# Kernel tuning notes

Measured on AMD Instinct MI355X. Metric: run time of the kernel, lower is better.

Reference implementation:

```python
import jax, jax.numpy as jnp
import numpy as np

N_NODES = 100000
N_EDGES = 1600000
D = 128        # in_dim == hidden_dim (forced by x_j + xe in message)
C = 64         # num_classes
G = 128        # number of graphs in the batch
BN_EPS = 1e-5


def setup_inputs() -> dict:
    key = jax.random.key(0)
    ks = jax.random.split(key, 14)
    s = 0.05
    inp = {
        "x": jax.random.normal(ks[0], (N_NODES, D), dtype=jnp.float32),
        "xe": jax.random.normal(ks[1], (N_EDGES, D), dtype=jnp.float32),
        "edge_index": jax.random.randint(ks[2], (2, N_EDGES), 0, N_NODES, dtype=jnp.int32),
        "batch": jnp.sort(jax.random.randint(ks[3], (N_NODES,), 0, G, dtype=jnp.int32)),
        # layer 0 MySAGEConv params
        "Wl0": jax.random.normal(ks[4], (D, D), dtype=jnp.float32) * s,
        "bl0": jnp.zeros((D,), dtype=jnp.float32),
        "Wr0": jax.random.normal(ks[5], (D, D), dtype=jnp.float32) * s,
        # layer 1 MySAGEConv params
        "Wl1": jax.random.normal(ks[6], (D, D), dtype=jnp.float32) * s,
        "bl1": jnp.zeros((D,), dtype=jnp.float32),
        "Wr1": jax.random.normal(ks[7], (D, D), dtype=jnp.float32) * s,
        # BatchNorm (only applied after non-final layers -> layer 0)
        "gamma0": jnp.ones((D,), dtype=jnp.float32),
        "beta0": jnp.zeros((D,), dtype=jnp.float32),
        # readout projection
        "Wp": jax.random.normal(ks[8], (C, D), dtype=jnp.float32) * s,
        "bp": jnp.zeros((C,), dtype=jnp.float32),
    }
    return inp


def _segment_mean(vals, idx, num_segments):
    s = jax.ops.segment_sum(vals, idx, num_segments=num_segments)
    cnt = jax.ops.segment_sum(jnp.ones((vals.shape[0],), vals.dtype), idx,
                              num_segments=num_segments)
    return s / jnp.clip(cnt, 1.0)[:, None]


def _my_sage_conv(h, xe, src, dst, Wl, bl, Wr):
    # message: relu(x_j + xe); aggregate: scatter-mean at dst; then lin_l + lin_r
    msg = jax.nn.relu(h[src] + xe)                       # [E, D]
    agg = _segment_mean(msg, dst, N_NODES)               # [N, D]
    return agg @ Wl.T + bl + h @ Wr.T


def _batchnorm_train(h, gamma, beta):
    mu = jnp.mean(h, axis=0)
    var = jnp.var(h, axis=0)
    return gamma * (h - mu) * jax.lax.rsqrt(var + BN_EPS) + beta


def reference(x, xe, edge_index, batch,
              Wl0, bl0, Wr0, Wl1, bl1, Wr1,
              gamma0, beta0, Wp, bp):
    src, dst = edge_index[0], edge_index[1]
    # layer 0: conv -> BN -> ReLU
    h = _my_sage_conv(x, xe, src, dst, Wl0, bl0, Wr0)
    h = jax.nn.relu(_batchnorm_train(h, gamma0, beta0))
    # layer 1 (last): conv only
    h = _my_sage_conv(h, xe, src, dst, Wl1, bl1, Wr1)
    # graph readout (global mean pool over pre-proj node features)
    g = _segment_mean(h, batch, G)                       # [G, D]
    # readout projection on nodes
    h = jax.nn.relu(h) @ Wp.T + bp                       # [N, C]
    return h, g
```

## Files before the change

kernel.cpp:

```cpp
#include <hip/hip_runtime.h>

#define N_NODES 100000
#define N_EDGES 1600000
#define DIM 128
#define NCLS 64
#define NG 128
#define BN_EPS 1e-5f

typedef __attribute__((ext_vector_type(8))) short s16x8;
typedef __attribute__((ext_vector_type(4))) float f32x4;
#define MFMA_BF16 __builtin_amdgcn_mfma_f32_16x16x32_bf16

__device__ __forceinline__ unsigned short f2b(float x) {
    unsigned u = __float_as_uint(x);
    return (unsigned short)((u + 0x7FFFu + ((u >> 16) & 1u)) >> 16);
}
__device__ __forceinline__ float b2f(unsigned short s) {
    return __uint_as_float(((unsigned)s) << 16);
}
__device__ __forceinline__ float4 bexp4(ushort4 u) {
    float4 f;
    f.x = b2f(u.x); f.y = b2f(u.y); f.z = b2f(u.z); f.w = b2f(u.w);
    return f;
}

__device__ __forceinline__ void f2hl8(float4 v0, float4 v1, s16x8& h8, s16x8& l8) {
    float vv[8] = {v0.x, v0.y, v0.z, v0.w, v1.x, v1.y, v1.z, v1.w};
#pragma unroll
    for (int i = 0; i < 8; ++i) {
        unsigned u = __float_as_uint(vv[i]);
        short h = (short)(u >> 16);
        float r = vv[i] - __uint_as_float(u & 0xFFFF0000u);
        short l = (short)(__float_as_uint(r) >> 16);
        h8[i] = h;
        l8[i] = l;
    }
}

__device__ __forceinline__ float4 relu4(float4 v) {
    v.x = fmaxf(v.x, 0.f); v.y = fmaxf(v.y, 0.f);
    v.z = fmaxf(v.z, 0.f); v.w = fmaxf(v.w, 0.f);
    return v;
}

__global__ void k_cvt(const float* __restrict__ in, unsigned short* __restrict__ out,
                      int n8) {
    int i = blockIdx.x * 256 + threadIdx.x;
    if (i >= n8) return;
    float4 a = reinterpret_cast<const float4*>(in)[(size_t)i * 2];
    float4 b = reinterpret_cast<const float4*>(in)[(size_t)i * 2 + 1];
    ushort4 oa, ob;
    oa.x = f2b(a.x); oa.y = f2b(a.y); oa.z = f2b(a.z); oa.w = f2b(a.w);
    ob.x = f2b(b.x); ob.y = f2b(b.y); ob.z = f2b(b.z); ob.w = f2b(b.w);
    reinterpret_cast<ushort4*>(out)[(size_t)i * 2] = oa;
    reinterpret_cast<ushort4*>(out)[(size_t)i * 2 + 1] = ob;
}

__global__ void k_hist(const int* __restrict__ dst, int* __restrict__ cnt) {
    int e = blockIdx.x * 256 + threadIdx.x;
    if (e < N_EDGES) atomicAdd(&cnt[dst[e]], 1);
}

__global__ void k_scan1(const int* __restrict__ cnt, int* __restrict__ rowptr,
                        int* __restrict__ bsums) {
    __shared__ int sd[1024];
    int tid = threadIdx.x;
    int i = blockIdx.x * 1024 + tid;
    int v = (i < N_NODES) ? cnt[i] : 0;
    sd[tid] = v;
    __syncthreads();
    for (int off = 1; off < 1024; off <<= 1) {
        int t2 = (tid >= off) ? sd[tid - off] : 0;
        __syncthreads();
        sd[tid] += t2;
        __syncthreads();
    }
    if (i < N_NODES) rowptr[i] = sd[tid] - v;
    if (tid == 1023) bsums[blockIdx.x] = sd[tid];
}

__global__ void k_scan2(int* __restrict__ bsums, int nb) {
    __shared__ int sd[128];
    int t = threadIdx.x;
    int v = (t < nb) ? bsums[t] : 0;
    sd[t] = v;
    __syncthreads();
    for (int off = 1; off < 128; off <<= 1) {
        int u = (t >= off) ? sd[t - off] : 0;
        __syncthreads();
        sd[t] += u;
        __syncthreads();
    }
    if (t < nb) bsums[t] = sd[t] - v;
}

__global__ void k_scan3(int* __restrict__ rowptr, const int* __restrict__ bsums,
                        int* __restrict__ wcur) {
    int i = blockIdx.x * 1024 + threadIdx.x;
    if (i < N_NODES) {
        int v = rowptr[i] + bsums[blockIdx.x];
        rowptr[i] = v;
        wcur[i] = v;
    }
    if (i == N_NODES - 1) rowptr[N_NODES] = N_EDGES;
}

__global__ void k_scatter(const int* __restrict__ src, const int* __restrict__ dst,
                          int* __restrict__ wcur, int2* __restrict__ esort) {
    int e = blockIdx.x * 256 + threadIdx.x;
    if (e < N_EDGES) {
        int d = dst[e];
        int p = atomicAdd(&wcur[d], 1);
        esort[p] = make_int2(e, src[e]);
    }
}

template <int MODE>
__global__ __launch_bounds__(256) void k_agg(
        const unsigned short* __restrict__ Fb, const float* __restrict__ xe,
        unsigned short* __restrict__ xe_s,
        const int* __restrict__ rowptr, const int2* __restrict__ esort,
        float* __restrict__ agg, const float* __restrict__ bnsc) {
    int wid = (blockIdx.x * 256 + threadIdx.x) >> 6;
    int lane = threadIdx.x & 63;
    if (wid >= N_NODES) return;
    int half = lane >> 5;
    int l = lane & 31;
    int p0 = rowptr[wid], p1 = rowptr[wid + 1];
    if (p0 == p1) {
        if (half == 0) {
            float4 z = make_float4(0.f, 0.f, 0.f, 0.f);
            *reinterpret_cast<float4*>(&agg[(size_t)wid * DIM + l * 4]) = z;
        }
        return;
    }
    float4 sc, sh;
    if (MODE != 0) {
        sc = *reinterpret_cast<const float4*>(&bnsc[l * 4]);
        sh = *reinterpret_cast<const float4*>(&bnsc[DIM + l * 4]);
    }
    float4 acc = make_float4(0.f, 0.f, 0.f, 0.f);
    for (int p = p0; p < p1; p += 8) {
#pragma unroll
        for (int j = 0; j < 4; ++j) {
            int q = p + j * 2 + half;
            int qc = min(q, p1 - 1);
            int2 es = esort[qc];
            float4 a = bexp4(*reinterpret_cast<const ushort4*>(
                &Fb[(size_t)es.y * DIM + l * 4]));
            float4 b;
            if (MODE == 1) {
                b = bexp4(*reinterpret_cast<const ushort4*>(
                    &xe_s[(size_t)qc * DIM + l * 4]));
            } else {
                b = *reinterpret_cast<const float4*>(
                    &xe[(size_t)es.x * DIM + l * 4]);
            }
            if (MODE != 0) {
                a.x = fmaxf(a.x * sc.x + sh.x, 0.f);
                a.y = fmaxf(a.y * sc.y + sh.y, 0.f);
                a.z = fmaxf(a.z * sc.z + sh.z, 0.f);
                a.w = fmaxf(a.w * sc.w + sh.w, 0.f);
            }
            if (q < p1) {
                if (MODE == 0) {
                    ushort4 o;
                    o.x = f2b(b.x); o.y = f2b(b.y);
                    o.z = f2b(b.z); o.w = f2b(b.w);
                    *reinterpret_cast<ushort4*>(&xe_s[(size_t)qc * DIM + l * 4]) = o;
                }
                acc.x += fmaxf(a.x + b.x, 0.f);
                acc.y += fmaxf(a.y + b.y, 0.f);
                acc.z += fmaxf(a.z + b.z, 0.f);
                acc.w += fmaxf(a.w + b.w, 0.f);
            }
        }
    }
    acc.x += __shfl_xor(acc.x, 32);
    acc.y += __shfl_xor(acc.y, 32);
    acc.z += __shfl_xor(acc.z, 32);
    acc.w += __shfl_xor(acc.w, 32);
    if (half == 0) {
        float s = 1.f / (float)(p1 - p0);
        acc.x *= s; acc.y *= s; acc.z *= s; acc.w *= s;
        *reinterpret_cast<float4*>(&agg[(size_t)wid * DIM + l * 4]) = acc;
    }
}

__global__ void k_wprep_all(const float* __restrict__ Wl0, const float* __restrict__ Wr0,
                            const float* __restrict__ Wl1, const float* __restrict__ Wr1,
                            const float* __restrict__ Wp,
                            short* __restrict__ fWl0h, short* __restrict__ fWl0l,
                            short* __restrict__ fWr0h, short* __restrict__ fWr0l,
                            short* __restrict__ fWl1h, short* __restrict__ fWl1l,
                            short* __restrict__ fWr1h, short* __restrict__ fWr1l,
                            short* __restrict__ fWph, short* __restrict__ fWpl) {
    int b = blockIdx.x;
    const float* W; short* hi; short* lo; int ct;
    if (b < 8)       { W = Wl0; hi = fWl0h; lo = fWl0l; ct = b; }
    else if (b < 16) { W = Wr0; hi = fWr0h; lo = fWr0l; ct = b - 8; }
    else if (b < 24) { W = Wl1; hi = fWl1h; lo = fWl1l; ct = b - 16; }
    else if (b < 32) { W = Wr1; hi = fWr1h; lo = fWr1l; ct = b - 24; }
    else             { W = Wp;  hi = fWph;  lo = fWpl;  ct = b - 32; }
    int tt = threadIdx.x;
    int lane = tt & 63, ks = (tt >> 6) & 3;
    int row = ct * 16 + (lane & 15);
    int k0 = ks * 32 + ((lane >> 4) << 3);
    float4 v0 = *reinterpret_cast<const float4*>(&W[(size_t)row * DIM + k0]);
    float4 v1 = *reinterpret_cast<const float4*>(&W[(size_t)row * DIM + k0 + 4]);
    s16x8 h8, l8;
    f2hl8(v0, v1, h8, l8);
    int t = ct * 256 + ks * 64 + lane;
    *reinterpret_cast<s16x8*>(&hi[(size_t)t * 8]) = h8;
    *reinterpret_cast<s16x8*>(&lo[(size_t)t * 8]) = l8;
}

__global__ __launch_bounds__(256) void k_gemm2(
        const float* __restrict__ A, const unsigned short* __restrict__ Bbf,
        const short* __restrict__ fW1h, const short* __restrict__ fW1l,
        const short* __restrict__ fW2h, const short* __restrict__ fW2l,
        const float* __restrict__ bias, float* __restrict__ OUTf,
        unsigned short* __restrict__ OUTb,
        float* __restrict__ bnacc, const float* __restrict__ bnsc,
        int doBN, int bnB) {
    int t = threadIdx.x, w = t >> 6, l = t & 63;
    int n0 = blockIdx.x * 128;
    int r = l & 15, kh = l >> 4;
    int row0 = n0 + w * 16 + r;
    int row1 = row0 + 64;
    int n_0 = min(row0, N_NODES - 1);
    int n_1 = min(row1, N_NODES - 1);

    f32x4 acc0[8], acc1[8];
#pragma unroll
    for (int ct = 0; ct < 8; ++ct) {
        acc0[ct] = (f32x4){0.f, 0.f, 0.f, 0.f};
        acc1[ct] = (f32x4){0.f, 0.f, 0.f, 0.f};
    }
    const s16x8* w1h = (const s16x8*)fW1h;
    const s16x8* w1l = (const s16x8*)fW1l;
    const s16x8* w2h = (const s16x8*)fW2h;
    const s16x8* w2l = (const s16x8*)fW2l;

#pragma unroll
    for (int ks = 0; ks < 4; ++ks) {
        int kb = ks * 32 + kh * 8;
        float4 va0 = *reinterpret_cast<const float4*>(&A[(size_t)n_0 * DIM + kb]);
        float4 va1 = *reinterpret_cast<const float4*>(&A[(size_t)n_0 * DIM + kb + 4]);
        float4 wa0 = *reinterpret_cast<const float4*>(&A[(size_t)n_1 * DIM + kb]);
        float4 wa1 = *reinterpret_cast<const float4*>(&A[(size_t)n_1 * DIM + kb + 4]);
        s16x8 b0 = *reinterpret_cast<const s16x8*>(&Bbf[(size_t)n_0 * DIM + kb]);
        s16x8 b1 = *reinterpret_cast<const s16x8*>(&Bbf[(size_t)n_1 * DIM + kb]);
        if (bnB) {
            float4 sc0 = *reinterpret_cast<const float4*>(&bnsc[kb]);
            float4 sh0 = *reinterpret_cast<const float4*>(&bnsc[DIM + kb]);
            float4 sc1 = *reinterpret_cast<const float4*>(&bnsc[kb + 4]);
            float4 sh1 = *reinterpret_cast<const float4*>(&bnsc[DIM + kb + 4]);
            float scv[8] = {sc0.x, sc0.y, sc0.z, sc0.w, sc1.x, sc1.y, sc1.z, sc1.w};
            float shv[8] = {sh0.x, sh0.y, sh0.z, sh0.w, sh1.x, sh1.y, sh1.z, sh1.w};
#pragma unroll
            for (int i = 0; i < 8; ++i) {
                float v = b2f((unsigned short)b0[i]);
                b0[i] = (short)f2b(fmaxf(v * scv[i] + shv[i], 0.f));
                v = b2f((unsigned short)b1[i]);
                b1[i] = (short)f2b(fmaxf(v * scv[i] + shv[i], 0.f));
            }
        }
        s16x8 a0h, a0l, a1h, a1l;
        f2hl8(va0, va1, a0h, a0l);
        f2hl8(wa0, wa1, a1h, a1l);
        int fb = ks * 64 + l;
#pragma unroll
        for (int ct = 0; ct < 8; ++ct) {
            int fi = ct * 256 + fb;
            s16x8 wh1 = w1h[fi], wl1 = w1l[fi];
            s16x8 wh2 = w2h[fi], wl2 = w2l[fi];
            acc0[ct] = MFMA_BF16(a0h, wh1, acc0[ct], 0, 0, 0);
            acc0[ct] = MFMA_BF16(a0h, wl1, acc0[ct], 0, 0, 0);
            acc0[ct] = MFMA_BF16(a0l, wh1, acc0[ct], 0, 0, 0);
            acc0[ct] = MFMA_BF16(b0, wh2, acc0[ct], 0, 0, 0);
            acc0[ct] = MFMA_BF16(b0, wl2, acc0[ct], 0, 0, 0);
            acc1[ct] = MFMA_BF16(a1h, wh1, acc1[ct], 0, 0, 0);
            acc1[ct] = MFMA_BF16(a1h, wl1, acc1[ct], 0, 0, 0);
            acc1[ct] = MFMA_BF16(a1l, wh1, acc1[ct], 0, 0, 0);
            acc1[ct] = MFMA_BF16(b1, wh2, acc1[ct], 0, 0, 0);
            acc1[ct] = MFMA_BF16(b1, wl2, acc1[ct], 0, 0, 0);
        }
    }

    float p1s[8], p2s[8];
    int col0 = l & 15;
    int nb0 = n0 + w * 16 + (kh << 2);
    int nb1 = nb0 + 64;
#pragma unroll
    for (int ct = 0; ct < 8; ++ct) {
        float bj = bias[ct * 16 + col0];
        float s1 = 0.f, s2 = 0.f;
#pragma unroll
        for (int rr = 0; rr < 4; ++rr) {
            int n = nb0 + rr;
            float h = acc0[ct][rr] + bj;
            if (n < N_NODES) {
                if (OUTb) OUTb[(size_t)n * DIM + ct * 16 + col0] = f2b(h);
                else      OUTf[(size_t)n * DIM + ct * 16 + col0] = h;
                s1 += h; s2 += h * h;
            }
            n = nb1 + rr;
            h = acc1[ct][rr] + bj;
            if (n < N_NODES) {
                if (OUTb) OUTb[(size_t)n * DIM + ct * 16 + col0] = f2b(h);
                else      OUTf[(size_t)n * DIM + ct * 16 + col0] = h;
                s1 += h; s2 += h * h;
            }
        }
        p1s[ct] = s1; p2s[ct] = s2;
    }
    if (doBN) {
        __shared__ float red1[512];
        __shared__ float red2[512];
#pragma unroll
        for (int ct = 0; ct < 8; ++ct) {
            p1s[ct] += __shfl_xor(p1s[ct], 16);
            p1s[ct] += __shfl_xor(p1s[ct], 32);
            p2s[ct] += __shfl_xor(p2s[ct], 16);
            p2s[ct] += __shfl_xor(p2s[ct], 32);
        }
        if (l < 16) {
#pragma unroll
            for (int ct = 0; ct < 8; ++ct) {
                red1[w * 128 + ct * 16 + l] = p1s[ct];
                red2[w * 128 + ct * 16 + l] = p2s[ct];
            }
        }
        __syncthreads();
        if (t < 128) {
            float s1 = red1[t] + red1[128 + t] + red1[256 + t] + red1[384 + t];
            float s2 = red2[t] + red2[128 + t] + red2[256 + t] + red2[384 + t];
            atomicAdd(&bnacc[t], s1);
            atomicAdd(&bnacc[128 + t], s2);
        }
    }
}

__global__ void k_bnfinal(const float* __restrict__ bnacc, const float* __restrict__ gamma,
                          const float* __restrict__ beta, float* __restrict__ bnsc) {
    int d = threadIdx.x;
    if (d < DIM) {
        float mu = bnacc[d] / (float)N_NODES;
        float var = bnacc[128 + d] / (float)N_NODES - mu * mu;
        float rstd = rsqrtf(var + BN_EPS);
        float sc = gamma[d] * rstd;
        bnsc[d] = sc;
        bnsc[128 + d] = beta[d] - mu * sc;
    }
}

__global__ void k_pool(const float* __restrict__ H1, const int* __restrict__ batch,
                       float* __restrict__ gout) {
    __shared__ float red[4][128];
    int g = blockIdx.x;
    int t = threadIdx.x;
    int d = t & 127;
    int sl = t >> 7;
    int lo = 0, hi = N_NODES;
    while (lo < hi) { int m = (lo + hi) >> 1; if (batch[m] < g) lo = m + 1; else hi = m; }
    int s = lo;
    lo = 0; hi = N_NODES;
    while (lo < hi) { int m = (lo + hi) >> 1; if (batch[m] < g + 1) lo = m + 1; else hi = m; }
    int e = lo;
    float sum = 0.f;
    for (int n = s + sl; n < e; n += 4) sum += H1[(size_t)n * DIM + d];
    red[sl][d] = sum;
    __syncthreads();
    if (t < 128) {
        float tot = red[0][d] + red[1][d] + red[2][d] + red[3][d];
        gout[g * DIM + d] = tot / (float)max(e - s, 1);
    }
}

__global__ __launch_bounds__(256) void k_proj(
        const float* __restrict__ H1, const short* __restrict__ fWph,
        const short* __restrict__ fWpl, const float* __restrict__ bp,
        float* __restrict__ OUT) {
    int t = threadIdx.x, w = t >> 6, l = t & 63;
    int n0 = blockIdx.x * 128;
    int r = l & 15, kh = l >> 4;
    int row0 = n0 + w * 16 + r;
    int row1 = row0 + 64;
    int n_0 = min(row0, N_NODES - 1);
    int n_1 = min(row1, N_NODES - 1);
    f32x4 acc0[4], acc1[4];
#pragma unroll
    for (int ct = 0; ct < 4; ++ct) {
        acc0[ct] = (f32x4){0.f, 0.f, 0.f, 0.f};
        acc1[ct] = (f32x4){0.f, 0.f, 0.f, 0.f};
    }
    const s16x8* wph = (const s16x8*)fWph;
    const s16x8* wpl = (const s16x8*)fWpl;
#pragma unroll
    for (int ks = 0; ks < 4; ++ks) {
        int kb = ks * 32 + kh * 8;
        float4 va0 = relu4(*reinterpret_cast<const float4*>(&H1[(size_t)n_0 * DIM + kb]));
        float4 va1 = relu4(*reinterpret_cast<const float4*>(&H1[(size_t)n_0 * DIM + kb + 4]));
        float4 wa0 = relu4(*reinterpret_cast<const float4*>(&H1[(size_t)n_1 * DIM + kb]));
        float4 wa1 = relu4(*reinterpret_cast<const float4*>(&H1[(size_t)n_1 * DIM + kb + 4]));
        s16x8 a0h, a0l, a1h, a1l;
        f2hl8(va0, va1, a0h, a0l);
        f2hl8(wa0, wa1, a1h, a1l);
        int fb = ks * 64 + l;
#pragma unroll
        for (int ct = 0; ct < 4; ++ct) {
            int fi = ct * 256 + fb;
            s16x8 wh = wph[fi], wl = wpl[fi];
            acc0[ct] = MFMA_BF16(a0h, wh, acc0[ct], 0, 0, 0);
            acc0[ct] = MFMA_BF16(a0h, wl, acc0[ct], 0, 0, 0);
            acc0[ct] = MFMA_BF16(a0l, wh, acc0[ct], 0, 0, 0);
            acc1[ct] = MFMA_BF16(a1h, wh, acc1[ct], 0, 0, 0);
            acc1[ct] = MFMA_BF16(a1h, wl, acc1[ct], 0, 0, 0);
            acc1[ct] = MFMA_BF16(a1l, wh, acc1[ct], 0, 0, 0);
        }
    }
    int col0 = l & 15;
    int nb0 = n0 + w * 16 + (kh << 2);
    int nb1 = nb0 + 64;
#pragma unroll
    for (int ct = 0; ct < 4; ++ct) {
        float bj = bp[ct * 16 + col0];
#pragma unroll
        for (int rr = 0; rr < 4; ++rr) {
            int n = nb0 + rr;
            if (n < N_NODES)
                OUT[(size_t)n * NCLS + ct * 16 + col0] = acc0[ct][rr] + bj;
            n = nb1 + rr;
            if (n < N_NODES)
                OUT[(size_t)n * NCLS + ct * 16 + col0] = acc1[ct][rr] + bj;
        }
    }
}

extern "C" void kernel_launch(void* const* d_in, const int* in_sizes, int n_in,
                              void* d_out, int out_size, void* d_ws, size_t ws_size,
                              hipStream_t stream) {
    (void)in_sizes; (void)n_in; (void)out_size;
    const float* x     = (const float*)d_in[0];
    const float* xe    = (const float*)d_in[1];
    const int*   eidx  = (const int*)d_in[2];
    const int*   batch = (const int*)d_in[3];
    const float* Wl0   = (const float*)d_in[4];
    const float* bl0   = (const float*)d_in[5];
    const float* Wr0   = (const float*)d_in[6];
    const float* Wl1   = (const float*)d_in[7];
    const float* bl1   = (const float*)d_in[8];
    const float* Wr1   = (const float*)d_in[9];
    const float* gamma0 = (const float*)d_in[10];
    const float* beta0  = (const float*)d_in[11];
    const float* Wp    = (const float*)d_in[12];
    const float* bp    = (const float*)d_in[13];
    const int* srcp = eidx;
    const int* dstp = eidx + N_EDGES;

    char* ws = (char*)d_ws;
    size_t off = 0;
    auto carve = [&](size_t bytes) {
        void* p = ws + off;
        off = (off + bytes + 255) & ~(size_t)255;
        return p;
    };
    int*   cnt    = (int*)carve((size_t)N_NODES * 4);
    int*   rowptr = (int*)carve((size_t)(N_NODES + 1) * 4);
    int*   wcur   = (int*)carve((size_t)N_NODES * 4);
    int*   bsums  = (int*)carve(128 * 4);
    float* bnacc  = (float*)carve(256 * 4);
    float* bnsc   = (float*)carve(256 * 4);
    int2*  esort  = (int2*)carve((size_t)N_EDGES * 8);
    float* AGG    = (float*)carve((size_t)N_NODES * DIM * 4);
    float* H1     = (float*)carve((size_t)N_NODES * DIM * 4);
    unsigned short* x_bf = (unsigned short*)carve((size_t)N_NODES * DIM * 2);
    unsigned short* H_bf = (unsigned short*)carve((size_t)N_NODES * DIM * 2);
    short* fWl0h = (short*)carve(16384 * 2);
    short* fWl0l = (short*)carve(16384 * 2);
    short* fWr0h = (short*)carve(16384 * 2);
    short* fWr0l = (short*)carve(16384 * 2);
    short* fWl1h = (short*)carve(16384 * 2);
    short* fWl1l = (short*)carve(16384 * 2);
    short* fWr1h = (short*)carve(16384 * 2);
    short* fWr1l = (short*)carve(16384 * 2);
    short* fWph  = (short*)carve(8192 * 2);
    short* fWpl  = (short*)carve(8192 * 2);

    size_t xes_bytes = (size_t)N_EDGES * DIM * 2;
    int seq = (off + xes_bytes + 256 <= ws_size) ? 1 : 0;
    unsigned short* xe_s = seq ? (unsigned short*)carve(xes_bytes) : nullptr;

    float* out_h = (float*)d_out;
    float* out_g = out_h + (size_t)N_NODES * NCLS;

    hipMemsetAsync(cnt, 0, (size_t)N_NODES * 4, stream);
    hipMemsetAsync(bnacc, 0, 256 * 4, stream);

    k_wprep_all<<<36, 256, 0, stream>>>(Wl0, Wr0, Wl1, Wr1, Wp,
                                        fWl0h, fWl0l, fWr0h, fWr0l,
                                        fWl1h, fWl1l, fWr1h, fWr1l,
                                        fWph, fWpl);
    k_cvt<<<(N_NODES * DIM / 8 + 255) / 256, 256, 0, stream>>>(x, x_bf,
                                                               N_NODES * DIM / 8);

    int nb = (N_NODES + 1023) / 1024;
    k_hist<<<(N_EDGES + 255) / 256, 256, 0, stream>>>(dstp, cnt);
    k_scan1<<<nb, 1024, 0, stream>>>(cnt, rowptr, bsums);
    k_scan2<<<1, 128, 0, stream>>>(bsums, nb);
    k_scan3<<<nb, 1024, 0, stream>>>(rowptr, bsums, wcur);
    k_scatter<<<(N_EDGES + 255) / 256, 256, 0, stream>>>(srcp, dstp, wcur, esort);

    int ablocks = (N_NODES * 64 + 255) / 256;
    int gblocks = (N_NODES + 127) / 128;

    if (seq)
        k_agg<0><<<ablocks, 256, 0, stream>>>(x_bf, xe, xe_s, rowptr, esort, AGG, bnsc);
    else
        k_agg<2><<<ablocks, 256, 0, stream>>>(x_bf, xe, nullptr, rowptr, esort, AGG, bnsc);
    k_gemm2<<<gblocks, 256, 0, stream>>>(AGG, x_bf, fWl0h, fWl0l, fWr0h, fWr0l,
                                         bl0, nullptr, H_bf, bnacc, bnsc, 1, 0);
    k_bnfinal<<<1, 128, 0, stream>>>(bnacc, gamma0, beta0, bnsc);

    if (seq)
        k_agg<1><<<ablocks, 256, 0, stream>>>(H_bf, xe, xe_s, rowptr, esort, AGG, bnsc);
    else
        k_agg<2><<<ablocks, 256, 0, stream>>>(H_bf, xe, nullptr, rowptr, esort, AGG, bnsc);
    k_gemm2<<<gblocks, 256, 0, stream>>>(AGG, H_bf, fWl1h, fWl1l, fWr1h, fWr1l,
                                         bl1, H1, nullptr, bnacc, bnsc, 0, 1);

    k_pool<<<NG, 512, 0, stream>>>(H1, batch, out_g);
    k_proj<<<gblocks, 256, 0, stream>>>(H1, fWph, fWpl, bp, out_h);
}
```

Measured before the change: 866.1 us.

## Store aggregates and final hidden features in bf16; fuse setup kernels

```diff
diff --git a/kernel.cpp b/kernel.cpp
--- a/kernel.cpp
+++ b/kernel.cpp
@@ -37,28 +37,50 @@
     }
 }
 
-__device__ __forceinline__ float4 relu4(float4 v) {
-    v.x = fmaxf(v.x, 0.f); v.y = fmaxf(v.y, 0.f);
-    v.z = fmaxf(v.z, 0.f); v.w = fmaxf(v.w, 0.f);
-    return v;
-}
-
-__global__ void k_cvt(const float* __restrict__ in, unsigned short* __restrict__ out,
-                      int n8) {
-    int i = blockIdx.x * 256 + threadIdx.x;
-    if (i >= n8) return;
-    float4 a = reinterpret_cast<const float4*>(in)[(size_t)i * 2];
-    float4 b = reinterpret_cast<const float4*>(in)[(size_t)i * 2 + 1];
-    ushort4 oa, ob;
-    oa.x = f2b(a.x); oa.y = f2b(a.y); oa.z = f2b(a.z); oa.w = f2b(a.w);
-    ob.x = f2b(b.x); ob.y = f2b(b.y); ob.z = f2b(b.z); ob.w = f2b(b.w);
-    reinterpret_cast<ushort4*>(out)[(size_t)i * 2] = oa;
-    reinterpret_cast<ushort4*>(out)[(size_t)i * 2 + 1] = ob;
-}
-
-__global__ void k_hist(const int* __restrict__ dst, int* __restrict__ cnt) {
-    int e = blockIdx.x * 256 + threadIdx.x;
-    if (e < N_EDGES) atomicAdd(&cnt[dst[e]], 1);
+__global__ __launch_bounds__(256) void k_mega0(
+        const float* __restrict__ Wl0, const float* __restrict__ Wr0,
+        const float* __restrict__ Wl1, const float* __restrict__ Wr1,
+        const float* __restrict__ Wp,
+        short* __restrict__ fWl0h, short* __restrict__ fWl0l,
+        short* __restrict__ fWr0h, short* __restrict__ fWr0l,
+        short* __restrict__ fWl1h, short* __restrict__ fWl1l,
+        short* __restrict__ fWr1h, short* __restrict__ fWr1l,
+        short* __restrict__ fWph, short* __restrict__ fWpl,
+        const float* __restrict__ x, unsigned short* __restrict__ x_bf,
+        const int* __restrict__ dst, int* __restrict__ cnt) {
+    int b = blockIdx.x;
+    if (b < 36) {
+        const float* W; short* hi; short* lo; int ct;
+        if (b < 8)       { W = Wl0; hi = fWl0h; lo = fWl0l; ct = b; }
+        else if (b < 16) { W = Wr0; hi = fWr0h; lo = fWr0l; ct = b - 8; }
+        else if (b < 24) { W = Wl1; hi = fWl1h; lo = fWl1l; ct = b - 16; }
+        else if (b < 32) { W = Wr1; hi = fWr1h; lo = fWr1l; ct = b - 24; }
+        else             { W = Wp;  hi = fWph;  lo = fWpl;  ct = b - 32; }
+        if (b >= 32 && ct >= 4) return;
+        int tt = threadIdx.x;
+        int lane = tt & 63, ks = (tt >> 6) & 3;
+        int row = ct * 16 + (lane & 15);
+        int k0 = ks * 32 + ((lane >> 4) << 3);
+        float4 v0 = *reinterpret_cast<const float4*>(&W[(size_t)row * DIM + k0]);
+        float4 v1 = *reinterpret_cast<const float4*>(&W[(size_t)row * DIM + k0 + 4]);
+        s16x8 h8, l8;
+        f2hl8(v0, v1, h8, l8);
+        int t = ct * 256 + ks * 64 + lane;
+        *reinterpret_cast<s16x8*>(&hi[(size_t)t * 8]) = h8;
+        *reinterpret_cast<s16x8*>(&lo[(size_t)t * 8]) = l8;
+    } else if (b < 36 + 6250) {
+        int i = (b - 36) * 256 + threadIdx.x;
+        float4 a = reinterpret_cast<const float4*>(x)[(size_t)i * 2];
+        float4 c = reinterpret_cast<const float4*>(x)[(size_t)i * 2 + 1];
+        ushort4 oa, ob;
+        oa.x = f2b(a.x); oa.y = f2b(a.y); oa.z = f2b(a.z); oa.w = f2b(a.w);
+        ob.x = f2b(c.x); ob.y = f2b(c.y); ob.z = f2b(c.z); ob.w = f2b(c.w);
+        reinterpret_cast<ushort4*>(x_bf)[(size_t)i * 2] = oa;
+        reinterpret_cast<ushort4*>(x_bf)[(size_t)i * 2 + 1] = ob;
+    } else {
+        int e = (b - 36 - 6250) * 256 + threadIdx.x;
+        atomicAdd(&cnt[dst[e]], 1);
+    }
 }
 
 __global__ void k_scan1(const int* __restrict__ cnt, int* __restrict__ rowptr,
@@ -120,7 +142,7 @@
         const unsigned short* __restrict__ Fb, const float* __restrict__ xe,
         unsigned short* __restrict__ xe_s,
         const int* __restrict__ rowptr, const int2* __restrict__ esort,
-        float* __restrict__ agg, const float* __restrict__ bnsc) {
+        unsigned short* __restrict__ agg, const float* __restrict__ bnsc) {
     int wid = (blockIdx.x * 256 + threadIdx.x) >> 6;
     int lane = threadIdx.x & 63;
     if (wid >= N_NODES) return;
@@ -129,8 +151,8 @@
     int p0 = rowptr[wid], p1 = rowptr[wid + 1];
     if (p0 == p1) {
         if (half == 0) {
-            float4 z = make_float4(0.f, 0.f, 0.f, 0.f);
-            *reinterpret_cast<float4*>(&agg[(size_t)wid * DIM + l * 4]) = z;
+            ushort4 z = make_ushort4(0, 0, 0, 0);
+            *reinterpret_cast<ushort4*>(&agg[(size_t)wid * DIM + l * 4]) = z;
         }
         return;
     }
@@ -182,45 +204,18 @@
     acc.w += __shfl_xor(acc.w, 32);
     if (half == 0) {
         float s = 1.f / (float)(p1 - p0);
-        acc.x *= s; acc.y *= s; acc.z *= s; acc.w *= s;
-        *reinterpret_cast<float4*>(&agg[(size_t)wid * DIM + l * 4]) = acc;
-    }
-}
-
-__global__ void k_wprep_all(const float* __restrict__ Wl0, const float* __restrict__ Wr0,
-                            const float* __restrict__ Wl1, const float* __restrict__ Wr1,
-                            const float* __restrict__ Wp,
-                            short* __restrict__ fWl0h, short* __restrict__ fWl0l,
-                            short* __restrict__ fWr0h, short* __restrict__ fWr0l,
-                            short* __restrict__ fWl1h, short* __restrict__ fWl1l,
-                            short* __restrict__ fWr1h, short* __restrict__ fWr1l,
-                            short* __restrict__ fWph, short* __restrict__ fWpl) {
-    int b = blockIdx.x;
-    const float* W; short* hi; short* lo; int ct;
-    if (b < 8)       { W = Wl0; hi = fWl0h; lo = fWl0l; ct = b; }
-    else if (b < 16) { W = Wr0; hi = fWr0h; lo = fWr0l; ct = b - 8; }
-    else if (b < 24) { W = Wl1; hi = fWl1h; lo = fWl1l; ct = b - 16; }
-    else if (b < 32) { W = Wr1; hi = fWr1h; lo = fWr1l; ct = b - 24; }
-    else             { W = Wp;  hi = fWph;  lo = fWpl;  ct = b - 32; }
-    int tt = threadIdx.x;
-    int lane = tt & 63, ks = (tt >> 6) & 3;
-    int row = ct * 16 + (lane & 15);
-    int k0 = ks * 32 + ((lane >> 4) << 3);
-    float4 v0 = *reinterpret_cast<const float4*>(&W[(size_t)row * DIM + k0]);
-    float4 v1 = *reinterpret_cast<const float4*>(&W[(size_t)row * DIM + k0 + 4]);
-    s16x8 h8, l8;
-    f2hl8(v0, v1, h8, l8);
-    int t = ct * 256 + ks * 64 + lane;
-    *reinterpret_cast<s16x8*>(&hi[(size_t)t * 8]) = h8;
-    *reinterpret_cast<s16x8*>(&lo[(size_t)t * 8]) = l8;
+        ushort4 o;
+        o.x = f2b(acc.x * s); o.y = f2b(acc.y * s);
+        o.z = f2b(acc.z * s); o.w = f2b(acc.w * s);
+        *reinterpret_cast<ushort4*>(&agg[(size_t)wid * DIM + l * 4]) = o;
+    }
 }
 
 __global__ __launch_bounds__(256) void k_gemm2(
-        const float* __restrict__ A, const unsigned short* __restrict__ Bbf,
+        const unsigned short* __restrict__ Abf, const unsigned short* __restrict__ Bbf,
         const short* __restrict__ fW1h, const short* __restrict__ fW1l,
         const short* __restrict__ fW2h, const short* __restrict__ fW2l,
-        const float* __restrict__ bias, float* __restrict__ OUTf,
-        unsigned short* __restrict__ OUTb,
+        const float* __restrict__ bias, unsigned short* __restrict__ OUTb,
         float* __restrict__ bnacc, const float* __restrict__ bnsc,
         int doBN, int bnB) {
     int t = threadIdx.x, w = t >> 6, l = t & 63;
@@ -245,10 +240,8 @@
 #pragma unroll
     for (int ks = 0; ks < 4; ++ks) {
         int kb = ks * 32 + kh * 8;
-        float4 va0 = *reinterpret_cast<const float4*>(&A[(size_t)n_0 * DIM + kb]);
-        float4 va1 = *reinterpret_cast<const float4*>(&A[(size_t)n_0 * DIM + kb + 4]);
-        float4 wa0 = *reinterpret_cast<const float4*>(&A[(size_t)n_1 * DIM + kb]);
-        float4 wa1 = *reinterpret_cast<const float4*>(&A[(size_t)n_1 * DIM + kb + 4]);
+        s16x8 a0 = *reinterpret_cast<const s16x8*>(&Abf[(size_t)n_0 * DIM + kb]);
+        s16x8 a1 = *reinterpret_cast<const s16x8*>(&Abf[(size_t)n_1 * DIM + kb]);
         s16x8 b0 = *reinterpret_cast<const s16x8*>(&Bbf[(size_t)n_0 * DIM + kb]);
         s16x8 b1 = *reinterpret_cast<const s16x8*>(&Bbf[(size_t)n_1 * DIM + kb]);
         if (bnB) {
@@ -266,23 +259,18 @@
                 b1[i] = (short)f2b(fmaxf(v * scv[i] + shv[i], 0.f));
             }
         }
-        s16x8 a0h, a0l, a1h, a1l;
-        f2hl8(va0, va1, a0h, a0l);
-        f2hl8(wa0, wa1, a1h, a1l);
         int fb = ks * 64 + l;
 #pragma unroll
         for (int ct = 0; ct < 8; ++ct) {
             int fi = ct * 256 + fb;
             s16x8 wh1 = w1h[fi], wl1 = w1l[fi];
             s16x8 wh2 = w2h[fi], wl2 = w2l[fi];
-            acc0[ct] = MFMA_BF16(a0h, wh1, acc0[ct], 0, 0, 0);
-            acc0[ct] = MFMA_BF16(a0h, wl1, acc0[ct], 0, 0, 0);
-            acc0[ct] = MFMA_BF16(a0l, wh1, acc0[ct], 0, 0, 0);
+            acc0[ct] = MFMA_BF16(a0, wh1, acc0[ct], 0, 0, 0);
+            acc0[ct] = MFMA_BF16(a0, wl1, acc0[ct], 0, 0, 0);
             acc0[ct] = MFMA_BF16(b0, wh2, acc0[ct], 0, 0, 0);
             acc0[ct] = MFMA_BF16(b0, wl2, acc0[ct], 0, 0, 0);
-            acc1[ct] = MFMA_BF16(a1h, wh1, acc1[ct], 0, 0, 0);
-            acc1[ct] = MFMA_BF16(a1h, wl1, acc1[ct], 0, 0, 0);
-            acc1[ct] = MFMA_BF16(a1l, wh1, acc1[ct], 0, 0, 0);
+            acc1[ct] = MFMA_BF16(a1, wh1, acc1[ct], 0, 0, 0);
+            acc1[ct] = MFMA_BF16(a1, wl1, acc1[ct], 0, 0, 0);
             acc1[ct] = MFMA_BF16(b1, wh2, acc1[ct], 0, 0, 0);
             acc1[ct] = MFMA_BF16(b1, wl2, acc1[ct], 0, 0, 0);
         }
@@ -301,15 +289,13 @@
             int n = nb0 + rr;
             float h = acc0[ct][rr] + bj;
             if (n < N_NODES) {
-                if (OUTb) OUTb[(size_t)n * DIM + ct * 16 + col0] = f2b(h);
-                else      OUTf[(size_t)n * DIM + ct * 16 + col0] = h;
+                OUTb[(size_t)n * DIM + ct * 16 + col0] = f2b(h);
                 s1 += h; s2 += h * h;
             }
             n = nb1 + rr;
             h = acc1[ct][rr] + bj;
             if (n < N_NODES) {
-                if (OUTb) OUTb[(size_t)n * DIM + ct * 16 + col0] = f2b(h);
-                else      OUTf[(size_t)n * DIM + ct * 16 + col0] = h;
+                OUTb[(size_t)n * DIM + ct * 16 + col0] = f2b(h);
                 s1 += h; s2 += h * h;
             }
         }
@@ -355,8 +341,8 @@
     }
 }
 
-__global__ void k_pool(const float* __restrict__ H1, const int* __restrict__ batch,
-                       float* __restrict__ gout) {
+__global__ void k_pool(const unsigned short* __restrict__ H1b,
+                       const int* __restrict__ batch, float* __restrict__ gout) {
     __shared__ float red[4][128];
     int g = blockIdx.x;
     int t = threadIdx.x;
@@ -369,7 +355,7 @@
     while (lo < hi) { int m = (lo + hi) >> 1; if (batch[m] < g + 1) lo = m + 1; else hi = m; }
     int e = lo;
     float sum = 0.f;
-    for (int n = s + sl; n < e; n += 4) sum += H1[(size_t)n * DIM + d];
+    for (int n = s + sl; n < e; n += 4) sum += b2f(H1b[(size_t)n * DIM + d]);
     red[sl][d] = sum;
     __syncthreads();
     if (t < 128) {
@@ -379,7 +365,7 @@
 }
 
 __global__ __launch_bounds__(256) void k_proj(
-        const float* __restrict__ H1, const short* __restrict__ fWph,
+        const unsigned short* __restrict__ H1b, const short* __restrict__ fWph,
         const short* __restrict__ fWpl, const float* __restrict__ bp,
         float* __restrict__ OUT) {
     int t = threadIdx.x, w = t >> 6, l = t & 63;
@@ -400,24 +386,23 @@
 #pragma unroll
     for (int ks = 0; ks < 4; ++ks) {
         int kb = ks * 32 + kh * 8;
-        float4 va0 = relu4(*reinterpret_cast<const float4*>(&H1[(size_t)n_0 * DIM + kb]));
-        float4 va1 = relu4(*reinterpret_cast<const float4*>(&H1[(size_t)n_0 * DIM + kb + 4]));
-        float4 wa0 = relu4(*reinterpret_cast<const float4*>(&H1[(size_t)n_1 * DIM + kb]));
-        float4 wa1 = relu4(*reinterpret_cast<const float4*>(&H1[(size_t)n_1 * DIM + kb + 4]));
-        s16x8 a0h, a0l, a1h, a1l;
-        f2hl8(va0, va1, a0h, a0l);
-        f2hl8(wa0, wa1, a1h, a1l);
+        s16x8 r0 = *reinterpret_cast<const s16x8*>(&H1b[(size_t)n_0 * DIM + kb]);
+        s16x8 r1 = *reinterpret_cast<const s16x8*>(&H1b[(size_t)n_1 * DIM + kb]);
+        s16x8 a0, a1;
+#pragma unroll
+        for (int i = 0; i < 8; ++i) {
+            a0[i] = r0[i] < 0 ? (short)0 : r0[i];
+            a1[i] = r1[i] < 0 ? (short)0 : r1[i];
+        }
         int fb = ks * 64 + l;
 #pragma unroll
         for (int ct = 0; ct < 4; ++ct) {
             int fi = ct * 256 + fb;
             s16x8 wh = wph[fi], wl = wpl[fi];
-            acc0[ct] = MFMA_BF16(a0h, wh, acc0[ct], 0, 0, 0);
-            acc0[ct] = MFMA_BF16(a0h, wl, acc0[ct], 0, 0, 0);
-            acc0[ct] = MFMA_BF16(a0l, wh, acc0[ct], 0, 0, 0);
-            acc1[ct] = MFMA_BF16(a1h, wh, acc1[ct], 0, 0, 0);
-            acc1[ct] = MFMA_BF16(a1h, wl, acc1[ct], 0, 0, 0);
-            acc1[ct] = MFMA_BF16(a1l, wh, acc1[ct], 0, 0, 0);
+            acc0[ct] = MFMA_BF16(a0, wh, acc0[ct], 0, 0, 0);
+            acc0[ct] = MFMA_BF16(a0, wl, acc0[ct], 0, 0, 0);
+            acc1[ct] = MFMA_BF16(a1, wh, acc1[ct], 0, 0, 0);
+            acc1[ct] = MFMA_BF16(a1, wl, acc1[ct], 0, 0, 0);
         }
     }
     int col0 = l & 15;
@@ -473,10 +458,10 @@
     float* bnacc  = (float*)carve(256 * 4);
     float* bnsc   = (float*)carve(256 * 4);
     int2*  esort  = (int2*)carve((size_t)N_EDGES * 8);
-    float* AGG    = (float*)carve((size_t)N_NODES * DIM * 4);
-    float* H1     = (float*)carve((size_t)N_NODES * DIM * 4);
+    unsigned short* AGGb = (unsigned short*)carve((size_t)N_NODES * DIM * 2);
     unsigned short* x_bf = (unsigned short*)carve((size_t)N_NODES * DIM * 2);
     unsigned short* H_bf = (unsigned short*)carve((size_t)N_NODES * DIM * 2);
+    unsigned short* H1b  = (unsigned short*)carve((size_t)N_NODES * DIM * 2);
     short* fWl0h = (short*)carve(16384 * 2);
     short* fWl0l = (short*)carve(16384 * 2);
     short* fWr0h = (short*)carve(16384 * 2);
@@ -498,15 +483,12 @@
     hipMemsetAsync(cnt, 0, (size_t)N_NODES * 4, stream);
     hipMemsetAsync(bnacc, 0, 256 * 4, stream);
 
-    k_wprep_all<<<36, 256, 0, stream>>>(Wl0, Wr0, Wl1, Wr1, Wp,
-                                        fWl0h, fWl0l, fWr0h, fWr0l,
-                                        fWl1h, fWl1l, fWr1h, fWr1l,
-                                        fWph, fWpl);
-    k_cvt<<<(N_NODES * DIM / 8 + 255) / 256, 256, 0, stream>>>(x, x_bf,
-                                                               N_NODES * DIM / 8);
+    k_mega0<<<36 + 6250 + 6250, 256, 0, stream>>>(
+        Wl0, Wr0, Wl1, Wr1, Wp,
+        fWl0h, fWl0l, fWr0h, fWr0l, fWl1h, fWl1l, fWr1h, fWr1l, fWph, fWpl,
+        x, x_bf, dstp, cnt);
 
     int nb = (N_NODES + 1023) / 1024;
-    k_hist<<<(N_EDGES + 255) / 256, 256, 0, stream>>>(dstp, cnt);
     k_scan1<<<nb, 1024, 0, stream>>>(cnt, rowptr, bsums);
     k_scan2<<<1, 128, 0, stream>>>(bsums, nb);
     k_scan3<<<nb, 1024, 0, stream>>>(rowptr, bsums, wcur);
@@ -516,20 +498,20 @@
     int gblocks = (N_NODES + 127) / 128;
 
     if (seq)
-        k_agg<0><<<ablocks, 256, 0, stream>>>(x_bf, xe, xe_s, rowptr, esort, AGG, bnsc);
+        k_agg<0><<<ablocks, 256, 0, stream>>>(x_bf, xe, xe_s, rowptr, esort, AGGb, bnsc);
     else
-        k_agg<2><<<ablocks, 256, 0, stream>>>(x_bf, xe, nullptr, rowptr, esort, AGG, bnsc);
-    k_gemm2<<<gblocks, 256, 0, stream>>>(AGG, x_bf, fWl0h, fWl0l, fWr0h, fWr0l,
-                                         bl0, nullptr, H_bf, bnacc, bnsc, 1, 0);
+        k_agg<2><<<ablocks, 256, 0, stream>>>(x_bf, xe, nullptr, rowptr, esort, AGGb, bnsc);
+    k_gemm2<<<gblocks, 256, 0, stream>>>(AGGb, x_bf, fWl0h, fWl0l, fWr0h, fWr0l,
+                                         bl0, H_bf, bnacc, bnsc, 1, 0);
     k_bnfinal<<<1, 128, 0, stream>>>(bnacc, gamma0, beta0, bnsc);
 
     if (seq)
-        k_agg<1><<<ablocks, 256, 0, stream>>>(H_bf, xe, xe_s, rowptr, esort, AGG, bnsc);
+        k_agg<1><<<ablocks, 256, 0, stream>>>(H_bf, xe, xe_s, rowptr, esort, AGGb, bnsc);
     else
-        k_agg<2><<<ablocks, 256, 0, stream>>>(H_bf, xe, nullptr, rowptr, esort, AGG, bnsc);
-    k_gemm2<<<gblocks, 256, 0, stream>>>(AGG, H_bf, fWl1h, fWl1l, fWr1h, fWr1l,
-                                         bl1, H1, nullptr, bnacc, bnsc, 0, 1);
-
-    k_pool<<<NG, 512, 0, stream>>>(H1, batch, out_g);
-    k_proj<<<gblocks, 256, 0, stream>>>(H1, fWph, fWpl, bp, out_h);
-}
+        k_agg<2><<<ablocks, 256, 0, stream>>>(H_bf, xe, nullptr, rowptr, esort, AGGb, bnsc);
+    k_gemm2<<<gblocks, 256, 0, stream>>>(AGGb, H_bf, fWl1h, fWl1l, fWr1h, fWr1l,
+                                         bl1, H1b, bnacc, bnsc, 0, 1);
+
+    k_pool<<<NG, 512, 0, stream>>>(H1b, batch, out_g);
+    k_proj<<<gblocks, 256, 0, stream>>>(H1b, fWph, fWpl, bp, out_h);
+}
```

Result: no change. 862.5 us (-0.4%).
